# Performance work log

Hardware: AMD Instinct MI355X
Metric: run time of the kernel (lower is better)

## Reference

```python
import jax, jax.numpy as jnp
import numpy as np

BETA = 0.25
TEMP = 0.5  # softmax temperature divisor used in Codebook.forward


def setup_inputs() -> dict:
    key = jax.random.key(0)
    k1, k2 = jax.random.split(key)
    B, C, H, W = 16, 512, 28, 28
    num_pq, K = 4, 2048
    d = C // num_pq  # 128
    z = jax.random.normal(k1, (B, C, H, W), dtype=jnp.float32)
    # nn.Embedding init: uniform(-1/K, 1/K), one codebook per product quantizer
    codebooks = jax.random.uniform(k2, (num_pq, K, d), dtype=jnp.float32,
                                   minval=-1.0 / K, maxval=1.0 / K)
    return {"z": z, "codebooks": codebooks}


def reference(z, codebooks):
    B, C, H, W = z.shape
    P, K, d = codebooks.shape  # P product quantizers, K codes, d = C // P
    N = B * H * W

    # torch.chunk(z, P, dim=1) then permute(0,2,3,1).view(-1, d) per chunk
    # -> (P, N, d)
    zc = z.reshape(B, P, d, H, W)
    zf = jnp.transpose(zc, (1, 0, 3, 4, 2)).reshape(P, N, d)

    # normalize == 'none': z_norm = z_flat, codebook_norm = codebook
    # pairwise squared distances: ||z||^2 + ||c||^2 - 2 z c^T  -> (P, N, K)
    dist = (jnp.sum(zf * zf, axis=-1, keepdims=True)
            + jnp.sum(codebooks * codebooks, axis=-1)[:, None, :]
            - 2.0 * jnp.einsum('pnd,pkd->pnk', zf, codebooks))

    idx = jnp.argmin(dist, axis=-1)                      # (P, N)
    prob = jax.nn.softmax(-dist / TEMP, axis=-1)         # (P, N, K)

    # use_weighted_sum == False: z_q = embedding lookup
    zq = codebooks[jnp.arange(P)[:, None], idx]          # (P, N, d)

    # losses: mean over P of per-quantizer MSE == global MSE (equal sizes)
    codebook_loss = jnp.mean((zq - jax.lax.stop_gradient(zf)) ** 2)
    commitment_loss = jnp.mean((zf - jax.lax.stop_gradient(zq)) ** 2)
    q_loss = codebook_loss + BETA * commitment_loss

    # straight-through estimator
    zq_st = zf + jax.lax.stop_gradient(zq - zf)

    # back to (B, C, H, W): (P,N,d)->(P,B,H,W,d)->(B,P,d,H,W)->(B,C,H,W)
    zq_out = jnp.transpose(zq_st.reshape(P, B, H, W, d),
                           (1, 0, 4, 2, 3)).reshape(B, C, H, W)

    # distance_prob concat along last dim: (N, P*K)
    distance_prob = jnp.transpose(prob, (1, 0, 2)).reshape(N, P * K)

    return zq_out, q_loss, distance_prob
```

## Files before the change

kernel.cpp:

```cpp
#include <hip/hip_runtime.h>

#define P_    4
#define K_    2048
#define D_    128
#define B_    16
#define HW_   784
#define N_    (B_ * HW_)
#define C_    512

#define OUT0_SZ   (B_ * C_ * HW_)
#define QLOSS_OFF OUT0_SZ
#define OUT2_OFF  (OUT0_SZ + 1)

typedef short  short8 __attribute__((ext_vector_type(8)));
typedef float  f32x4  __attribute__((ext_vector_type(4)));

__device__ __forceinline__ short f2bf(float x) {
    union { float f; unsigned u; } a; a.f = x;
    unsigned r = a.u + 0x7FFF + ((a.u >> 16) & 1);
    return (short)(r >> 16);
}

__global__ __launch_bounds__(256) void vq_prep(const float* __restrict__ cb,
                                               short* __restrict__ cbb,
                                               float* __restrict__ cnorm) {
    int wave = threadIdx.x >> 6;
    int lane = threadIdx.x & 63;
    int row  = blockIdx.x * 4 + wave;
    const float* src = cb + (size_t)row * D_;
    float2 v = *(const float2*)(src + lane * 2);
    cbb[(size_t)row * D_ + lane * 2 + 0] = f2bf(v.x);
    cbb[(size_t)row * D_ + lane * 2 + 1] = f2bf(v.y);
    float s = v.x * v.x + v.y * v.y;
    #pragma unroll
    for (int m = 1; m < 64; m <<= 1) s += __shfl_xor(s, m, 64);
    if (lane == 0) cnorm[row] = s;
}

__global__ __launch_bounds__(512, 4) void vq_main(const float* __restrict__ z,
                                                  const short* __restrict__ cbb,
                                                  const float* __restrict__ cnorm,
                                                  int*   __restrict__ idx_out,
                                                  float* __restrict__ out2) {
    __shared__ short As[16][136];
    __shared__ float wsum[8][16];
    __shared__ float wmax[8][16];
    __shared__ int   wmidx[8][16];

    const int bx  = blockIdx.x;
    const int p   = bx / (N_ / 16);
    const int nt  = bx % (N_ / 16);
    const int b   = nt / 49;
    const int hw0 = (nt % 49) * 16;
    const int n0  = nt * 16;

    {
        int t  = threadIdx.x;
        int k  = t >> 2;
        int q4 = t & 3;
        const float* src = z + ((size_t)b * C_ + p * D_ + k) * HW_ + hw0 + q4 * 4;
        float4 v = *(const float4*)src;
        int r0 = q4 * 4;
        As[r0 + 0][k] = f2bf(v.x);  As[r0 + 1][k] = f2bf(v.y);
        As[r0 + 2][k] = f2bf(v.z);  As[r0 + 3][k] = f2bf(v.w);
    }
    __syncthreads();

    const int wave = threadIdx.x >> 6;
    const int lane = threadIdx.x & 63;
    const int llo  = lane & 15;
    const int lhi  = lane >> 4;

    short8 af[4];
    #pragma unroll
    for (int s = 0; s < 4; s++)
        af[s] = *(const short8*)&As[llo][s * 32 + lhi * 8];

    const short* bptr = cbb + ((size_t)(p * K_ + wave * 256 + llo) * D_ + lhi * 8);

    f32x4 acc[16];
    #pragma unroll
    for (int ct = 0; ct < 16; ct++) {
        const short* bp = bptr + (size_t)ct * 16 * D_;
        short8 b0 = *(const short8*)(bp +  0);
        short8 b1 = *(const short8*)(bp + 32);
        short8 b2 = *(const short8*)(bp + 64);
        short8 b3 = *(const short8*)(bp + 96);
        f32x4 a = {0.f, 0.f, 0.f, 0.f};
        a = __builtin_amdgcn_mfma_f32_16x16x32_bf16(af[0], b0, a, 0, 0, 0);
        a = __builtin_amdgcn_mfma_f32_16x16x32_bf16(af[1], b1, a, 0, 0, 0);
        a = __builtin_amdgcn_mfma_f32_16x16x32_bf16(af[2], b2, a, 0, 0, 0);
        a = __builtin_amdgcn_mfma_f32_16x16x32_bf16(af[3], b3, a, 0, 0, 0);
        acc[ct] = a;
    }

    float rs[4] = {0.f, 0.f, 0.f, 0.f};
    float mx[4] = {-1e30f, -1e30f, -1e30f, -1e30f};
    int   mi[4] = {0, 0, 0, 0};
    const float* cn = cnorm + p * K_ + wave * 256 + llo;
    #pragma unroll
    for (int ct = 0; ct < 16; ct++) {
        float c = cn[ct * 16];
        #pragma unroll
        for (int r = 0; r < 4; r++) {
            float s = 4.0f * acc[ct][r] - 2.0f * c;
            float e = __expf(s);
            acc[ct][r] = e;
            rs[r] += e;
            if (e > mx[r]) { mx[r] = e; mi[r] = wave * 256 + ct * 16 + llo; }
        }
    }
    #pragma unroll
    for (int m = 1; m < 16; m <<= 1) {
        #pragma unroll
        for (int r = 0; r < 4; r++) {
            rs[r] += __shfl_xor(rs[r], m, 64);
            float om = __shfl_xor(mx[r], m, 64);
            int   oi = __shfl_xor(mi[r], m, 64);
            if (om > mx[r] || (om == mx[r] && oi < mi[r])) { mx[r] = om; mi[r] = oi; }
        }
    }
    if (llo == 0) {
        #pragma unroll
        for (int r = 0; r < 4; r++) {
            int row = lhi * 4 + r;
            wsum[wave][row]  = rs[r];
            wmax[wave][row]  = mx[r];
            wmidx[wave][row] = mi[r];
        }
    }
    __syncthreads();

    float inv[4];
    #pragma unroll
    for (int r = 0; r < 4; r++) {
        int row = lhi * 4 + r;
        float s = 0.f;
        #pragma unroll
        for (int w2 = 0; w2 < 8; w2++) s += wsum[w2][row];
        inv[r] = 1.0f / s;
    }
    if (threadIdx.x < 16) {
        int row = threadIdx.x;
        float m0 = wmax[0][row]; int i0 = wmidx[0][row];
        #pragma unroll
        for (int w2 = 1; w2 < 8; w2++) {
            float mm = wmax[w2][row]; int ii = wmidx[w2][row];
            if (mm > m0 || (mm == m0 && ii < i0)) { m0 = mm; i0 = ii; }
        }
        idx_out[p * N_ + n0 + row] = i0;
    }

    float* obase = out2 + (size_t)(n0 + lhi * 4) * (P_ * K_) + p * K_ + wave * 256 + llo;
    #pragma unroll
    for (int ct = 0; ct < 16; ct++) {
        #pragma unroll
        for (int r = 0; r < 4; r++) {
            obase[(size_t)r * (P_ * K_) + ct * 16] = acc[ct][r] * inv[r];
        }
    }
}

__global__ __launch_bounds__(256) void vq_gather(const float* __restrict__ z,
                                                 const float* __restrict__ cb,
                                                 const int*   __restrict__ idx,
                                                 float* __restrict__ out0,
                                                 float* __restrict__ qloss) {
    const int bp  = blockIdx.x;
    const int b   = bp >> 2;
    const int p   = bp & 3;
    const int dd0 = blockIdx.y * 8;
    const int t   = threadIdx.x;
    float loss = 0.f;
    for (int hw = t; hw < HW_; hw += 256) {
        int iv = idx[p * N_ + b * HW_ + hw];
        const float* crow = cb + ((size_t)(p * K_ + iv)) * D_ + dd0;
        float4 c0 = *(const float4*)crow;
        float4 c1 = *(const float4*)(crow + 4);
        float cv[8] = {c0.x, c0.y, c0.z, c0.w, c1.x, c1.y, c1.z, c1.w};
        size_t zoff = ((size_t)b * C_ + p * D_ + dd0) * HW_ + hw;
        #pragma unroll
        for (int j = 0; j < 8; j++) {
            float zv = z[zoff + (size_t)j * HW_];
            out0[zoff + (size_t)j * HW_] = cv[j];
            float dlt = cv[j] - zv;
            loss += dlt * dlt;
        }
    }
    #pragma unroll
    for (int m = 1; m < 64; m <<= 1) loss += __shfl_xor(loss, m, 64);
    __shared__ float ls[4];
    int wave = t >> 6, lane = t & 63;
    if (lane == 0) ls[wave] = loss;
    __syncthreads();
    if (t == 0) {
        float tot = ls[0] + ls[1] + ls[2] + ls[3];
        atomicAdd(qloss, tot * (1.25f / (float)(P_ * (size_t)N_ * D_)));
    }
}

extern "C" void kernel_launch(void* const* d_in, const int* in_sizes, int n_in,
                              void* d_out, int out_size, void* d_ws, size_t ws_size,
                              hipStream_t stream) {
    const float* z  = (const float*)d_in[0];
    const float* cb = (const float*)d_in[1];
    float* out = (float*)d_out;

    int*   ws_idx   = (int*)d_ws;
    float* ws_cnorm = (float*)((char*)d_ws + (256 << 10));
    short* ws_cbb   = (short*)((char*)d_ws + (512 << 10));

    vq_prep<<<(P_ * K_) / 4, 256, 0, stream>>>(cb, ws_cbb, ws_cnorm);
    vq_main<<<P_ * (N_ / 16), 512, 0, stream>>>(z, ws_cbb, ws_cnorm, ws_idx,
                                                out + OUT2_OFF);
    hipMemsetAsync(out + QLOSS_OFF, 0, sizeof(float), stream);
    vq_gather<<<dim3(64, 16), 256, 0, stream>>>(z, cb, ws_idx, out,
                                                out + QLOSS_OFF);
}
```

Measured before the change: 671.9 us.

## Stage softmax output through LDS for coalesced row stores; widen gather tiles

The main kernel writes normalized probabilities into a shared-memory buffer four rows at a time, then stores each full row with 16-byte vector writes instead of strided per-lane scalar stores. This targets poor write coalescing on the large distance-probability output. The gather kernel now processes 32 channels per block and splits HW into halves, reducing redundant index and codebook loads. The cost is 32 KB more LDS per block and extra barriers, which may reduce occupancy.

```diff
diff --git a/kernel.cpp b/kernel.cpp
--- a/kernel.cpp
+++ b/kernel.cpp
@@ -46,6 +46,7 @@
     __shared__ float wsum[8][16];
     __shared__ float wmax[8][16];
     __shared__ int   wmidx[8][16];
+    __shared__ float ps[4][2048];
 
     const int bx  = blockIdx.x;
     const int p   = bx / (N_ / 16);
@@ -151,12 +152,27 @@
         idx_out[p * N_ + n0 + row] = i0;
     }
 
-    float* obase = out2 + (size_t)(n0 + lhi * 4) * (P_ * K_) + p * K_ + wave * 256 + llo;
-    #pragma unroll
-    for (int ct = 0; ct < 16; ct++) {
-        #pragma unroll
-        for (int r = 0; r < 4; r++) {
-            obase[(size_t)r * (P_ * K_) + ct * 16] = acc[ct][r] * inv[r];
+    #pragma unroll
+    for (int g = 0; g < 4; g++) {
+        __syncthreads();
+        if (lhi == g) {
+            #pragma unroll
+            for (int ct = 0; ct < 16; ct++) {
+                #pragma unroll
+                for (int r = 0; r < 4; r++)
+                    ps[r][wave * 256 + ct * 16 + llo] = acc[ct][r] * inv[r];
+            }
+        }
+        __syncthreads();
+        {
+            int row = threadIdx.x >> 7;
+            int c4  = (threadIdx.x & 127) * 4;
+            float* orow = out2 + (size_t)(n0 + g * 4 + row) * (P_ * K_) + p * K_;
+            #pragma unroll
+            for (int k = 0; k < 4; k++) {
+                f32x4 v = *(const f32x4*)&ps[row][c4 + k * 512];
+                *(f32x4*)(orow + c4 + k * 512) = v;
+            }
         }
     }
 }
@@ -166,24 +182,28 @@
                                                  const int*   __restrict__ idx,
                                                  float* __restrict__ out0,
                                                  float* __restrict__ qloss) {
-    const int bp  = blockIdx.x;
-    const int b   = bp >> 2;
-    const int p   = bp & 3;
-    const int dd0 = blockIdx.y * 8;
-    const int t   = threadIdx.x;
+    const int gx   = blockIdx.x;
+    const int b    = gx >> 3;
+    const int p    = (gx >> 1) & 3;
+    const int half = gx & 1;
+    const int dd0  = blockIdx.y * 32;
+    const int t    = threadIdx.x;
+    const int hwend = half * 392 + 392;
+
     float loss = 0.f;
-    for (int hw = t; hw < HW_; hw += 256) {
+    for (int hw = half * 392 + t; hw < hwend; hw += 256) {
         int iv = idx[p * N_ + b * HW_ + hw];
         const float* crow = cb + ((size_t)(p * K_ + iv)) * D_ + dd0;
-        float4 c0 = *(const float4*)crow;
-        float4 c1 = *(const float4*)(crow + 4);
-        float cv[8] = {c0.x, c0.y, c0.z, c0.w, c1.x, c1.y, c1.z, c1.w};
+        f32x4 c[8];
+        #pragma unroll
+        for (int q = 0; q < 8; q++) c[q] = *(const f32x4*)(crow + q * 4);
         size_t zoff = ((size_t)b * C_ + p * D_ + dd0) * HW_ + hw;
         #pragma unroll
-        for (int j = 0; j < 8; j++) {
+        for (int j = 0; j < 32; j++) {
+            float cv = c[j >> 2][j & 3];
             float zv = z[zoff + (size_t)j * HW_];
-            out0[zoff + (size_t)j * HW_] = cv[j];
-            float dlt = cv[j] - zv;
+            out0[zoff + (size_t)j * HW_] = cv;
+            float dlt = cv - zv;
             loss += dlt * dlt;
         }
     }
@@ -214,6 +234,6 @@
     vq_main<<<P_ * (N_ / 16), 512, 0, stream>>>(z, ws_cbb, ws_cnorm, ws_idx,
                                                 out + OUT2_OFF);
     hipMemsetAsync(out + QLOSS_OFF, 0, sizeof(float), stream);
-    vq_gather<<<dim3(64, 16), 256, 0, stream>>>(z, cb, ws_idx, out,
+    vq_gather<<<dim3(128, 4), 256, 0, stream>>>(z, cb, ws_idx, out,
                                                 out + QLOSS_OFF);
 }
```

New measurement: 640.1 us. 4.7% less time.
